# Kernel tuning notes

Hardware: AMD Instinct MI355X
Metric: run time of the kernel (lower is better)

Reference implementation:

```python
import jax, jax.numpy as jnp
import numpy as np

N = 2048   # nodes
E = 65536  # edges (avg degree 32)
F = 7      # node_feature_dim
S = 32     # state_dim
L = 16     # latent_dim
R = 3      # message passing rounds


def setup_inputs() -> dict:
    key = jax.random.key(0)
    ks = jax.random.split(key, 12)
    g = lambda k, shape, s: (jax.random.normal(k, shape, jnp.float32) * s)
    return dict(
        x=g(ks[0], (N, F), 1.0),
        edge_index=jax.random.randint(ks[1], (2, E), 0, N, dtype=jnp.int32),
        # input_net Linear(F->S)
        W_in=g(ks[2], (F, S), 0.3), b_in=jnp.zeros((S,), jnp.float32),
        # message nets: R x Linear(S->S)
        W_msg=g(ks[3], (R, S, S), 0.15), b_msg=jnp.zeros((R, S), jnp.float32),
        # GRU cells: R x (weight_ih, weight_hh) stored (in, 3*S) with torch gate order r,z,n
        W_ih=g(ks[4], (R, S, 3 * S), 0.15), W_hh=g(ks[5], (R, S, 3 * S), 0.15),
        b_ih=jnp.zeros((R, 3 * S), jnp.float32), b_hh=jnp.zeros((R, 3 * S), jnp.float32),
        # mu / logstd heads Linear(S->L)
        W_mu=g(ks[6], (S, L), 0.15), b_mu=jnp.zeros((L,), jnp.float32),
        W_ls=g(ks[7], (S, L), 0.15), b_ls=jnp.zeros((L,), jnp.float32),
        # decoder: Linear(2L->L), ReLU, Linear(L->1)
        W_d1=g(ks[8], (2 * L, L), 0.2), b_d1=jnp.zeros((L,), jnp.float32),
        W_d2=g(ks[9], (L, 1), 0.2), b_d2=jnp.zeros((1,), jnp.float32),
    )


def reference(x, edge_index, W_in, b_in, W_msg, b_msg, W_ih, W_hh, b_ih, b_hh,
              W_mu, b_mu, W_ls, b_ls, W_d1, b_d1, W_d2, b_d2):
    src, dst = edge_index[0], edge_index[1]
    # encoder
    state = jax.nn.relu(x @ W_in + b_in)  # [N, S]
    for r in range(R):
        message = jax.nn.relu(state @ W_msg[r] + b_msg[r])          # [N, S]
        aggregated = jax.ops.segment_sum(jnp.take(message, src, axis=0), dst,
                                         num_segments=N)            # [N, S]
        # GRUCell(aggregated, state), torch gate order: r, z, n
        gx = aggregated @ W_ih[r] + b_ih[r]                         # [N, 3S]
        gh = state @ W_hh[r] + b_hh[r]                              # [N, 3S]
        xr, xz, xn = jnp.split(gx, 3, axis=-1)
        hr, hz, hn = jnp.split(gh, 3, axis=-1)
        rg = jax.nn.sigmoid(xr + hr)
        zg = jax.nn.sigmoid(xz + hz)
        ng = jnp.tanh(xn + rg * hn)
        new_h = (1.0 - zg) * ng + zg * state
        state = state + new_h
    mu = state @ W_mu + b_mu        # [N, L]
    logstd = state @ W_ls + b_ls    # [N, L]
    # eval-mode reparameterize: z = mu
    z = mu
    # decode: Linear on concat([z_i, z_j]) == z_i @ W_d1[:L] + z_j @ W_d1[L:]
    a = z @ W_d1[:L]   # [N, L] contribution of row latent
    b = z @ W_d1[L:]   # [N, L] contribution of col latent
    h = jax.nn.relu(a[:, None, :] + b[None, :, :] + b_d1)  # [N, N, L]
    adj_logits = (h @ W_d2)[..., 0] + b_d2[0]              # [N, N]
    adj_logits = (adj_logits + adj_logits.T) / 2.0
    adj_recon = jax.nn.sigmoid(adj_logits)
    return (adj_recon, mu, logstd)
```

## Files before the change

kernel.cpp:

```cpp
#include <hip/hip_runtime.h>
#include <math.h>

#define NN 2048
#define EE 65536
#define FF 7
#define SS 32
#define LL 16
#define BKT 64
#define OCAP 4096

__device__ __forceinline__ float fsig(float x) { return 1.f / (1.f + __expf(-x)); }
__device__ __forceinline__ float ftanh(float x) { return 1.f - 2.f / (__expf(2.f * x) + 1.f); }

__global__ void k_enc(const float* __restrict__ x,
                      const float* __restrict__ W_in, const float* __restrict__ b_in,
                      const float* __restrict__ Wm, const float* __restrict__ bm,
                      float* __restrict__ st_out, float* __restrict__ msgA,
                      float* __restrict__ msgB,
                      int* __restrict__ cnt, int* __restrict__ ocnt,
                      int* __restrict__ bucket) {
    int gid = blockIdx.x * 256 + threadIdx.x;
    bucket[gid] = NN;
    bucket[gid + 65536] = NN;
    if (gid < NN) cnt[gid] = 0;
    if (gid == 0) *ocnt = 0;
    if (gid < SS) { msgA[NN * SS + gid] = 0.f; msgB[NN * SS + gid] = 0.f; }

    int n = gid >> 5, s = gid & 31;
    const float* xr = x + n * FF;
    float acc = b_in[s];
#pragma unroll
    for (int k = 0; k < FF; k++) acc += xr[k] * W_in[k * SS + s];
    float st = fmaxf(acc, 0.f);
    st_out[n * SS + s] = st;
    float m = bm[s];
#pragma unroll
    for (int k = 0; k < SS; k++) m += __shfl(st, k, 32) * Wm[k * SS + s];
    msgA[n * SS + s] = fmaxf(m, 0.f);
}

__global__ void k_bucket(const int* __restrict__ ei, int* __restrict__ cnt,
                         int* __restrict__ ocnt, int* __restrict__ olist,
                         int* __restrict__ bucket) {
    int e = blockIdx.x * 256 + threadIdx.x;
    int src = ei[e], dst = ei[EE + e];
    int slot = atomicAdd(&cnt[dst], 1);
    if (slot < BKT) bucket[dst * BKT + slot] = src;
    else {
        int oi = atomicAdd(ocnt, 1);
        if (oi < OCAP) { olist[2 * oi] = src; olist[2 * oi + 1] = dst; }
    }
}

__device__ __forceinline__ float gather_gru(int n, int s,
        const int* __restrict__ cnt, const int* __restrict__ bucket,
        const int* __restrict__ ocnt, const int* __restrict__ olist,
        const float* __restrict__ msg_in, const float* __restrict__ st_in,
        const float* __restrict__ Wih, const float* __restrict__ Whh,
        const float* __restrict__ bih, const float* __restrict__ bhh) {
    const int* bk = bucket + n * BKT;
    int i0 = bk[s], i1 = bk[SS + s];
    float acc = 0.f;
#pragma unroll
    for (int k = 0; k < 32; k++) acc += msg_in[__shfl(i0, k, 32) * SS + s];
#pragma unroll
    for (int k = 0; k < 32; k++) acc += msg_in[__shfl(i1, k, 32) * SS + s];
    int deg = cnt[n];
    if (deg > BKT) {
        int oc = *ocnt; if (oc > OCAP) oc = OCAP;
        for (int i = 0; i < oc; i++)
            if (olist[2 * i + 1] == n) acc += msg_in[olist[2 * i] * SS + s];
    }
    float h0 = st_in[n * SS + s];
    float xr = bih[s], xz = bih[SS + s], xn = bih[2 * SS + s];
    float hr = bhh[s], hz = bhh[SS + s], hn = bhh[2 * SS + s];
#pragma unroll
    for (int k = 0; k < SS; k++) {
        float av = __shfl(acc, k, 32);
        float hv = __shfl(h0, k, 32);
        const float* wi = Wih + k * 3 * SS;
        const float* wh = Whh + k * 3 * SS;
        xr += av * wi[s];
        xz += av * wi[SS + s];
        xn += av * wi[2 * SS + s];
        hr += hv * wh[s];
        hz += hv * wh[SS + s];
        hn += hv * wh[2 * SS + s];
    }
    float rg = fsig(xr + hr);
    float zg = fsig(xz + hz);
    float ng = ftanh(xn + rg * hn);
    return h0 + (1.f - zg) * ng + zg * h0;
}

__global__ void k_round(const int* __restrict__ cnt, const int* __restrict__ bucket,
                        const int* __restrict__ ocnt, const int* __restrict__ olist,
                        const float* __restrict__ msg_in, const float* __restrict__ st_in,
                        const float* __restrict__ Wih, const float* __restrict__ Whh,
                        const float* __restrict__ bih, const float* __restrict__ bhh,
                        const float* __restrict__ Wm, const float* __restrict__ bm,
                        float* __restrict__ st_out, float* __restrict__ msg_out) {
    int gid = blockIdx.x * 256 + threadIdx.x;
    int n = gid >> 5, s = gid & 31;
    float st = gather_gru(n, s, cnt, bucket, ocnt, olist, msg_in, st_in,
                          Wih, Whh, bih, bhh);
    st_out[n * SS + s] = st;
    float mv = bm[s];
#pragma unroll
    for (int k = 0; k < SS; k++) mv += __shfl(st, k, 32) * Wm[k * SS + s];
    msg_out[n * SS + s] = fmaxf(mv, 0.f);
}

__global__ void k_final(const int* __restrict__ cnt, const int* __restrict__ bucket,
                        const int* __restrict__ ocnt, const int* __restrict__ olist,
                        const float* __restrict__ msg_in, const float* __restrict__ st_in,
                        const float* __restrict__ Wih, const float* __restrict__ Whh,
                        const float* __restrict__ bih, const float* __restrict__ bhh,
                        const float* __restrict__ W_mu, const float* __restrict__ b_mu,
                        const float* __restrict__ W_ls, const float* __restrict__ b_ls,
                        const float* __restrict__ W_d1, const float* __restrict__ b_d1,
                        float* __restrict__ out_mu, float* __restrict__ out_ls,
                        float* __restrict__ Abuf, float* __restrict__ Bbuf) {
    int gid = blockIdx.x * 256 + threadIdx.x;
    int n = gid >> 5, s = gid & 31;
    float st = gather_gru(n, s, cnt, bucket, ocnt, olist, msg_in, st_in,
                          Wih, Whh, bih, bhh);
    int l = s & 15;
    const float* W = (s < 16) ? W_mu : W_ls;
    float v = (s < 16) ? b_mu[l] : b_ls[l];
#pragma unroll
    for (int k = 0; k < SS; k++) v += __shfl(st, k, 32) * W[k * LL + l];
    if (s < 16) out_mu[n * LL + l] = v; else out_ls[n * LL + l] = v;
    const float* Wd = W_d1 + ((s < 16) ? 0 : LL * LL);
    float ab = (s < 16) ? b_d1[l] : 0.f;
#pragma unroll
    for (int k = 0; k < LL; k++) ab += __shfl(v, k, 32) * Wd[k * LL + l];
    if (s < 16) Abuf[n * LL + l] = ab; else Bbuf[n * LL + l] = ab;
}

__global__ __launch_bounds__(256) void dec_kernel(const float* __restrict__ Abuf,
                                                  const float* __restrict__ Bbuf,
                                                  const float* __restrict__ W_d2,
                                                  const float* __restrict__ b_d2,
                                                  float* __restrict__ out) {
    __shared__ float ldsAj[LL * 64];
    __shared__ float ldsBj[LL * 64];
    __shared__ float ldsT[64 * 65];
    int t = blockIdx.x;
    int bi = (int)((65.f - sqrtf(4225.f - 8.f * (float)t)) * 0.5f);
    if (bi < 0) bi = 0;
    if (bi > 31) bi = 31;
    while (bi > 0 && (65 * bi - bi * bi) / 2 > t) bi--;
    while (bi < 31 && (65 * (bi + 1) - (bi + 1) * (bi + 1)) / 2 <= t) bi++;
    int bj = bi + (t - (65 * bi - bi * bi) / 2);
    int i0 = bi * 64, j0 = bj * 64;
    int tid = threadIdx.x;

    {
        int jr = tid >> 2, q = tid & 3;
        float4 va = ((const float4*)(Abuf + (size_t)(j0 + jr) * LL))[q];
        float4 vb = ((const float4*)(Bbuf + (size_t)(j0 + jr) * LL))[q];
        int l4 = q * 4;
        ldsAj[(l4 + 0) * 64 + jr] = va.x; ldsAj[(l4 + 1) * 64 + jr] = va.y;
        ldsAj[(l4 + 2) * 64 + jr] = va.z; ldsAj[(l4 + 3) * 64 + jr] = va.w;
        ldsBj[(l4 + 0) * 64 + jr] = vb.x; ldsBj[(l4 + 1) * 64 + jr] = vb.y;
        ldsBj[(l4 + 2) * 64 + jr] = vb.z; ldsBj[(l4 + 3) * 64 + jr] = vb.w;
    }
    __syncthreads();

    int jo = tid & 63;
    int ig = tid >> 6;
    float aj[LL], bjr[LL], w[LL];
#pragma unroll
    for (int l = 0; l < LL; l++) {
        aj[l] = ldsAj[l * 64 + jo];
        bjr[l] = ldsBj[l * 64 + jo];
        w[l] = W_d2[l];
    }
    float bd2 = b_d2[0];
    int j = j0 + jo;

#pragma unroll 2
    for (int ii = 0; ii < 16; ii++) {
        int i = i0 + ig * 16 + ii;
        const float4* Ai4 = (const float4*)(Abuf + (size_t)i * LL);
        const float4* Bi4 = (const float4*)(Bbuf + (size_t)i * LL);
        float4 a0 = Ai4[0], a1 = Ai4[1], a2 = Ai4[2], a3 = Ai4[3];
        float4 b0 = Bi4[0], b1 = Bi4[1], b2 = Bi4[2], b3 = Bi4[3];
        float ai[LL] = {a0.x, a0.y, a0.z, a0.w, a1.x, a1.y, a1.z, a1.w,
                        a2.x, a2.y, a2.z, a2.w, a3.x, a3.y, a3.z, a3.w};
        float bi_[LL] = {b0.x, b0.y, b0.z, b0.w, b1.x, b1.y, b1.z, b1.w,
                         b2.x, b2.y, b2.z, b2.w, b3.x, b3.y, b3.z, b3.w};
        float accij = 0.f, accji = 0.f;
#pragma unroll
        for (int l = 0; l < LL; l++) {
            accij += w[l] * fmaxf(ai[l] + bjr[l], 0.f);
            accji += w[l] * fmaxf(aj[l] + bi_[l], 0.f);
        }
        float logit = 0.5f * (accij + accji) + bd2;
        float p = 1.f / (1.f + __expf(-logit));
        out[(size_t)i * NN + j] = p;
        ldsT[jo * 65 + ig * 16 + ii] = p;
    }

    if (bi != bj) {
        __syncthreads();
        int jj = tid >> 2, qi = tid & 3;
        float v[16];
#pragma unroll
        for (int m = 0; m < 16; m++) v[m] = ldsT[jj * 65 + qi * 16 + m];
        float4* dst = (float4*)(out + (size_t)(j0 + jj) * NN + i0 + qi * 16);
#pragma unroll
        for (int q4 = 0; q4 < 4; q4++)
            dst[q4] = make_float4(v[4 * q4], v[4 * q4 + 1], v[4 * q4 + 2], v[4 * q4 + 3]);
    }
}

extern "C" void kernel_launch(void* const* d_in, const int* in_sizes, int n_in,
                              void* d_out, int out_size, void* d_ws, size_t ws_size,
                              hipStream_t stream) {
    const float* x    = (const float*)d_in[0];
    const int*   ei   = (const int*)d_in[1];
    const float* W_in = (const float*)d_in[2];
    const float* b_in = (const float*)d_in[3];
    const float* W_msg = (const float*)d_in[4];
    const float* b_msg = (const float*)d_in[5];
    const float* W_ih = (const float*)d_in[6];
    const float* W_hh = (const float*)d_in[7];
    const float* b_ih = (const float*)d_in[8];
    const float* b_hh = (const float*)d_in[9];
    const float* W_mu = (const float*)d_in[10];
    const float* b_mu = (const float*)d_in[11];
    const float* W_ls = (const float*)d_in[12];
    const float* b_ls = (const float*)d_in[13];
    const float* W_d1 = (const float*)d_in[14];
    const float* b_d1 = (const float*)d_in[15];
    const float* W_d2 = (const float*)d_in[16];
    const float* b_d2 = (const float*)d_in[17];

    float* ws = (float*)d_ws;
    float* stA  = ws;
    float* stB  = stA + NN * SS;
    float* msgA = stB + NN * SS;
    float* msgB = msgA + (NN + 1) * SS;
    float* Abuf = msgB + (NN + 1) * SS;
    float* Bbuf = Abuf + NN * LL;
    int* cnt    = (int*)(Bbuf + NN * LL);
    int* ocnt   = cnt + NN;
    int* olist  = ocnt + 1;
    int* bucket = olist + 2 * OCAP;

    float* out_adj = (float*)d_out;
    float* out_mu  = out_adj + (size_t)NN * NN;
    float* out_ls  = out_mu + NN * LL;

    k_enc<<<256, 256, 0, stream>>>(x, W_in, b_in, W_msg, b_msg,
                                   stA, msgA, msgB, cnt, ocnt, bucket);
    k_bucket<<<EE / 256, 256, 0, stream>>>(ei, cnt, ocnt, olist, bucket);

    k_round<<<256, 256, 0, stream>>>(
        cnt, bucket, ocnt, olist, msgA, stA, W_ih, W_hh, b_ih, b_hh,
        W_msg + 1 * SS * SS, b_msg + 1 * SS, stB, msgB);
    k_round<<<256, 256, 0, stream>>>(
        cnt, bucket, ocnt, olist, msgB, stB,
        W_ih + SS * 3 * SS, W_hh + SS * 3 * SS, b_ih + 3 * SS, b_hh + 3 * SS,
        W_msg + 2 * SS * SS, b_msg + 2 * SS, stA, msgA);
    k_final<<<256, 256, 0, stream>>>(
        cnt, bucket, ocnt, olist, msgA, stA,
        W_ih + 2 * SS * 3 * SS, W_hh + 2 * SS * 3 * SS,
        b_ih + 2 * 3 * SS, b_hh + 2 * 3 * SS,
        W_mu, b_mu, W_ls, b_ls, W_d1, b_d1,
        out_mu, out_ls, Abuf, Bbuf);

    dec_kernel<<<528, 256, 0, stream>>>(Abuf, Bbuf, W_d2, b_d2, out_adj);
}
```

Measured before the change: 56.11 us.

## Fuse all stages into one cooperative kernel with grid syncs

Replaces six separate kernel launches with a single cooperative kernel of 256 blocks that uses grid-wide syncs between the encoder, edge bucketing, the three GRU rounds and the decoder. The decoder now loops over its 528 tiles with a stride of 256 blocks. Bucket slots are no longer pre-filled with a sentinel that points at a zero row. Instead, gather reads are masked by node degree, which also removes the extra zero row from the message buffers. The aim is to cut launch gaps and inter-kernel drain. The cost is grid-sync overhead, and the decoder phase has fewer blocks than tiles, so parallelism there is reduced.

```diff
diff --git a/kernel.cpp b/kernel.cpp
--- a/kernel.cpp
+++ b/kernel.cpp
@@ -1,5 +1,8 @@
 #include <hip/hip_runtime.h>
+#include <hip/hip_cooperative_groups.h>
 #include <math.h>
+
+namespace cg = cooperative_groups;
 
 #define NN 2048
 #define EE 65536
@@ -9,63 +12,41 @@
 #define BKT 64
 #define OCAP 4096
 
+struct Params {
+    const float *x; const int *ei;
+    const float *W_in, *b_in, *W_msg, *b_msg, *W_ih, *W_hh, *b_ih, *b_hh;
+    const float *W_mu, *b_mu, *W_ls, *b_ls, *W_d1, *b_d1, *W_d2, *b_d2;
+    float *stA, *stB, *msgA, *msgB, *Abuf, *Bbuf;
+    int *cnt, *ocnt, *olist, *bucket;
+    float *out_adj, *out_mu, *out_ls;
+};
+
 __device__ __forceinline__ float fsig(float x) { return 1.f / (1.f + __expf(-x)); }
 __device__ __forceinline__ float ftanh(float x) { return 1.f - 2.f / (__expf(2.f * x) + 1.f); }
 
-__global__ void k_enc(const float* __restrict__ x,
-                      const float* __restrict__ W_in, const float* __restrict__ b_in,
-                      const float* __restrict__ Wm, const float* __restrict__ bm,
-                      float* __restrict__ st_out, float* __restrict__ msgA,
-                      float* __restrict__ msgB,
-                      int* __restrict__ cnt, int* __restrict__ ocnt,
-                      int* __restrict__ bucket) {
-    int gid = blockIdx.x * 256 + threadIdx.x;
-    bucket[gid] = NN;
-    bucket[gid + 65536] = NN;
-    if (gid < NN) cnt[gid] = 0;
-    if (gid == 0) *ocnt = 0;
-    if (gid < SS) { msgA[NN * SS + gid] = 0.f; msgB[NN * SS + gid] = 0.f; }
-
-    int n = gid >> 5, s = gid & 31;
-    const float* xr = x + n * FF;
-    float acc = b_in[s];
-#pragma unroll
-    for (int k = 0; k < FF; k++) acc += xr[k] * W_in[k * SS + s];
-    float st = fmaxf(acc, 0.f);
-    st_out[n * SS + s] = st;
-    float m = bm[s];
-#pragma unroll
-    for (int k = 0; k < SS; k++) m += __shfl(st, k, 32) * Wm[k * SS + s];
-    msgA[n * SS + s] = fmaxf(m, 0.f);
-}
-
-__global__ void k_bucket(const int* __restrict__ ei, int* __restrict__ cnt,
-                         int* __restrict__ ocnt, int* __restrict__ olist,
-                         int* __restrict__ bucket) {
-    int e = blockIdx.x * 256 + threadIdx.x;
-    int src = ei[e], dst = ei[EE + e];
-    int slot = atomicAdd(&cnt[dst], 1);
-    if (slot < BKT) bucket[dst * BKT + slot] = src;
-    else {
-        int oi = atomicAdd(ocnt, 1);
-        if (oi < OCAP) { olist[2 * oi] = src; olist[2 * oi + 1] = dst; }
-    }
-}
-
-__device__ __forceinline__ float gather_gru(int n, int s,
-        const int* __restrict__ cnt, const int* __restrict__ bucket,
-        const int* __restrict__ ocnt, const int* __restrict__ olist,
-        const float* __restrict__ msg_in, const float* __restrict__ st_in,
-        const float* __restrict__ Wih, const float* __restrict__ Whh,
-        const float* __restrict__ bih, const float* __restrict__ bhh) {
+__device__ __forceinline__ float gather_gru(int n, int s, int deg,
+        const int* bucket, const int* ocnt, const int* olist,
+        const float* msg_in, const float* st_in,
+        const float* Wih, const float* Whh,
+        const float* bih, const float* bhh) {
     const int* bk = bucket + n * BKT;
     int i0 = bk[s], i1 = bk[SS + s];
     float acc = 0.f;
 #pragma unroll
-    for (int k = 0; k < 32; k++) acc += msg_in[__shfl(i0, k, 32) * SS + s];
-#pragma unroll
-    for (int k = 0; k < 32; k++) acc += msg_in[__shfl(i1, k, 32) * SS + s];
-    int deg = cnt[n];
+    for (int k = 0; k < 32; k++) {
+        int bsrc = __shfl(i0, k, 32);
+        int src = (k < deg) ? bsrc : 0;
+        float v = msg_in[src * SS + s];
+        acc += (k < deg) ? v : 0.f;
+    }
+#pragma unroll
+    for (int k = 0; k < 32; k++) {
+        int kk = 32 + k;
+        int bsrc = __shfl(i1, k, 32);
+        int src = (kk < deg) ? bsrc : 0;
+        float v = msg_in[src * SS + s];
+        acc += (kk < deg) ? v : 0.f;
+    }
     if (deg > BKT) {
         int oc = *ocnt; if (oc > OCAP) oc = OCAP;
         for (int i = 0; i < oc; i++)
@@ -93,184 +74,204 @@
     return h0 + (1.f - zg) * ng + zg * h0;
 }
 
-__global__ void k_round(const int* __restrict__ cnt, const int* __restrict__ bucket,
-                        const int* __restrict__ ocnt, const int* __restrict__ olist,
-                        const float* __restrict__ msg_in, const float* __restrict__ st_in,
-                        const float* __restrict__ Wih, const float* __restrict__ Whh,
-                        const float* __restrict__ bih, const float* __restrict__ bhh,
-                        const float* __restrict__ Wm, const float* __restrict__ bm,
-                        float* __restrict__ st_out, float* __restrict__ msg_out) {
-    int gid = blockIdx.x * 256 + threadIdx.x;
-    int n = gid >> 5, s = gid & 31;
-    float st = gather_gru(n, s, cnt, bucket, ocnt, olist, msg_in, st_in,
-                          Wih, Whh, bih, bhh);
-    st_out[n * SS + s] = st;
-    float mv = bm[s];
-#pragma unroll
-    for (int k = 0; k < SS; k++) mv += __shfl(st, k, 32) * Wm[k * SS + s];
-    msg_out[n * SS + s] = fmaxf(mv, 0.f);
-}
-
-__global__ void k_final(const int* __restrict__ cnt, const int* __restrict__ bucket,
-                        const int* __restrict__ ocnt, const int* __restrict__ olist,
-                        const float* __restrict__ msg_in, const float* __restrict__ st_in,
-                        const float* __restrict__ Wih, const float* __restrict__ Whh,
-                        const float* __restrict__ bih, const float* __restrict__ bhh,
-                        const float* __restrict__ W_mu, const float* __restrict__ b_mu,
-                        const float* __restrict__ W_ls, const float* __restrict__ b_ls,
-                        const float* __restrict__ W_d1, const float* __restrict__ b_d1,
-                        float* __restrict__ out_mu, float* __restrict__ out_ls,
-                        float* __restrict__ Abuf, float* __restrict__ Bbuf) {
-    int gid = blockIdx.x * 256 + threadIdx.x;
-    int n = gid >> 5, s = gid & 31;
-    float st = gather_gru(n, s, cnt, bucket, ocnt, olist, msg_in, st_in,
-                          Wih, Whh, bih, bhh);
-    int l = s & 15;
-    const float* W = (s < 16) ? W_mu : W_ls;
-    float v = (s < 16) ? b_mu[l] : b_ls[l];
-#pragma unroll
-    for (int k = 0; k < SS; k++) v += __shfl(st, k, 32) * W[k * LL + l];
-    if (s < 16) out_mu[n * LL + l] = v; else out_ls[n * LL + l] = v;
-    const float* Wd = W_d1 + ((s < 16) ? 0 : LL * LL);
-    float ab = (s < 16) ? b_d1[l] : 0.f;
-#pragma unroll
-    for (int k = 0; k < LL; k++) ab += __shfl(v, k, 32) * Wd[k * LL + l];
-    if (s < 16) Abuf[n * LL + l] = ab; else Bbuf[n * LL + l] = ab;
-}
-
-__global__ __launch_bounds__(256) void dec_kernel(const float* __restrict__ Abuf,
-                                                  const float* __restrict__ Bbuf,
-                                                  const float* __restrict__ W_d2,
-                                                  const float* __restrict__ b_d2,
-                                                  float* __restrict__ out) {
+__global__ void __launch_bounds__(256) fused(Params p) {
+    cg::grid_group grid = cg::this_grid();
     __shared__ float ldsAj[LL * 64];
     __shared__ float ldsBj[LL * 64];
     __shared__ float ldsT[64 * 65];
-    int t = blockIdx.x;
-    int bi = (int)((65.f - sqrtf(4225.f - 8.f * (float)t)) * 0.5f);
-    if (bi < 0) bi = 0;
-    if (bi > 31) bi = 31;
-    while (bi > 0 && (65 * bi - bi * bi) / 2 > t) bi--;
-    while (bi < 31 && (65 * (bi + 1) - (bi + 1) * (bi + 1)) / 2 <= t) bi++;
-    int bj = bi + (t - (65 * bi - bi * bi) / 2);
-    int i0 = bi * 64, j0 = bj * 64;
+
     int tid = threadIdx.x;
-
-    {
-        int jr = tid >> 2, q = tid & 3;
-        float4 va = ((const float4*)(Abuf + (size_t)(j0 + jr) * LL))[q];
-        float4 vb = ((const float4*)(Bbuf + (size_t)(j0 + jr) * LL))[q];
-        int l4 = q * 4;
-        ldsAj[(l4 + 0) * 64 + jr] = va.x; ldsAj[(l4 + 1) * 64 + jr] = va.y;
-        ldsAj[(l4 + 2) * 64 + jr] = va.z; ldsAj[(l4 + 3) * 64 + jr] = va.w;
-        ldsBj[(l4 + 0) * 64 + jr] = vb.x; ldsBj[(l4 + 1) * 64 + jr] = vb.y;
-        ldsBj[(l4 + 2) * 64 + jr] = vb.z; ldsBj[(l4 + 3) * 64 + jr] = vb.w;
-    }
-    __syncthreads();
-
-    int jo = tid & 63;
-    int ig = tid >> 6;
-    float aj[LL], bjr[LL], w[LL];
-#pragma unroll
-    for (int l = 0; l < LL; l++) {
-        aj[l] = ldsAj[l * 64 + jo];
-        bjr[l] = ldsBj[l * 64 + jo];
-        w[l] = W_d2[l];
-    }
-    float bd2 = b_d2[0];
-    int j = j0 + jo;
+    int gid = blockIdx.x * 256 + tid;
+    int n = gid >> 5, s = gid & 31;
+
+    {
+        const float* xr = p.x + n * FF;
+        float acc = p.b_in[s];
+#pragma unroll
+        for (int k = 0; k < FF; k++) acc += xr[k] * p.W_in[k * SS + s];
+        float st = fmaxf(acc, 0.f);
+        p.stA[n * SS + s] = st;
+        float m = p.b_msg[s];
+#pragma unroll
+        for (int k = 0; k < SS; k++) m += __shfl(st, k, 32) * p.W_msg[k * SS + s];
+        p.msgA[n * SS + s] = fmaxf(m, 0.f);
+        if (gid < NN) p.cnt[gid] = 0;
+        if (gid == 0) *p.ocnt = 0;
+    }
+    grid.sync();
+
+    {
+        int e = gid;
+        int src = p.ei[e], dst = p.ei[EE + e];
+        int slot = atomicAdd(&p.cnt[dst], 1);
+        if (slot < BKT) p.bucket[dst * BKT + slot] = src;
+        else {
+            int oi = atomicAdd(p.ocnt, 1);
+            if (oi < OCAP) { p.olist[2 * oi] = src; p.olist[2 * oi + 1] = dst; }
+        }
+    }
+    grid.sync();
+
+    int deg = p.cnt[n];
+
+    {
+        float st = gather_gru(n, s, deg, p.bucket, p.ocnt, p.olist, p.msgA, p.stA,
+                              p.W_ih, p.W_hh, p.b_ih, p.b_hh);
+        p.stB[n * SS + s] = st;
+        const float* Wm = p.W_msg + 1 * SS * SS;
+        const float* bm = p.b_msg + 1 * SS;
+        float mv = bm[s];
+#pragma unroll
+        for (int k = 0; k < SS; k++) mv += __shfl(st, k, 32) * Wm[k * SS + s];
+        p.msgB[n * SS + s] = fmaxf(mv, 0.f);
+    }
+    grid.sync();
+
+    {
+        float st = gather_gru(n, s, deg, p.bucket, p.ocnt, p.olist, p.msgB, p.stB,
+                              p.W_ih + SS * 3 * SS, p.W_hh + SS * 3 * SS,
+                              p.b_ih + 3 * SS, p.b_hh + 3 * SS);
+        p.stA[n * SS + s] = st;
+        const float* Wm = p.W_msg + 2 * SS * SS;
+        const float* bm = p.b_msg + 2 * SS;
+        float mv = bm[s];
+#pragma unroll
+        for (int k = 0; k < SS; k++) mv += __shfl(st, k, 32) * Wm[k * SS + s];
+        p.msgA[n * SS + s] = fmaxf(mv, 0.f);
+    }
+    grid.sync();
+
+    {
+        float st = gather_gru(n, s, deg, p.bucket, p.ocnt, p.olist, p.msgA, p.stA,
+                              p.W_ih + 2 * SS * 3 * SS, p.W_hh + 2 * SS * 3 * SS,
+                              p.b_ih + 2 * 3 * SS, p.b_hh + 2 * 3 * SS);
+        int l = s & 15;
+        const float* W = (s < 16) ? p.W_mu : p.W_ls;
+        float v = (s < 16) ? p.b_mu[l] : p.b_ls[l];
+#pragma unroll
+        for (int k = 0; k < SS; k++) v += __shfl(st, k, 32) * W[k * LL + l];
+        if (s < 16) p.out_mu[n * LL + l] = v; else p.out_ls[n * LL + l] = v;
+        const float* Wd = p.W_d1 + ((s < 16) ? 0 : LL * LL);
+        float ab = (s < 16) ? p.b_d1[l] : 0.f;
+#pragma unroll
+        for (int k = 0; k < LL; k++) ab += __shfl(v, k, 32) * Wd[k * LL + l];
+        if (s < 16) p.Abuf[n * LL + l] = ab; else p.Bbuf[n * LL + l] = ab;
+    }
+    grid.sync();
+
+    float w[LL];
+#pragma unroll
+    for (int l = 0; l < LL; l++) w[l] = p.W_d2[l];
+    float bd2 = p.b_d2[0];
+
+    for (int t = blockIdx.x; t < 528; t += 256) {
+        __syncthreads();
+        int bi = (int)((65.f - sqrtf(4225.f - 8.f * (float)t)) * 0.5f);
+        if (bi < 0) bi = 0;
+        if (bi > 31) bi = 31;
+        while (bi > 0 && (65 * bi - bi * bi) / 2 > t) bi--;
+        while (bi < 31 && (65 * (bi + 1) - (bi + 1) * (bi + 1)) / 2 <= t) bi++;
+        int bj = bi + (t - (65 * bi - bi * bi) / 2);
+        int i0 = bi * 64, j0 = bj * 64;
+
+        {
+            int jr = tid >> 2, q = tid & 3;
+            float4 va = ((const float4*)(p.Abuf + (size_t)(j0 + jr) * LL))[q];
+            float4 vb = ((const float4*)(p.Bbuf + (size_t)(j0 + jr) * LL))[q];
+            int l4 = q * 4;
+            ldsAj[(l4 + 0) * 64 + jr] = va.x; ldsAj[(l4 + 1) * 64 + jr] = va.y;
+            ldsAj[(l4 + 2) * 64 + jr] = va.z; ldsAj[(l4 + 3) * 64 + jr] = va.w;
+            ldsBj[(l4 + 0) * 64 + jr] = vb.x; ldsBj[(l4 + 1) * 64 + jr] = vb.y;
+            ldsBj[(l4 + 2) * 64 + jr] = vb.z; ldsBj[(l4 + 3) * 64 + jr] = vb.w;
+        }
+        __syncthreads();
+
+        int jo = tid & 63;
+        int ig = tid >> 6;
+        float aj[LL], bjr[LL];
+#pragma unroll
+        for (int l = 0; l < LL; l++) {
+            aj[l] = ldsAj[l * 64 + jo];
+            bjr[l] = ldsBj[l * 64 + jo];
+        }
+        int j = j0 + jo;
 
 #pragma unroll 2
-    for (int ii = 0; ii < 16; ii++) {
-        int i = i0 + ig * 16 + ii;
-        const float4* Ai4 = (const float4*)(Abuf + (size_t)i * LL);
-        const float4* Bi4 = (const float4*)(Bbuf + (size_t)i * LL);
-        float4 a0 = Ai4[0], a1 = Ai4[1], a2 = Ai4[2], a3 = Ai4[3];
-        float4 b0 = Bi4[0], b1 = Bi4[1], b2 = Bi4[2], b3 = Bi4[3];
-        float ai[LL] = {a0.x, a0.y, a0.z, a0.w, a1.x, a1.y, a1.z, a1.w,
-                        a2.x, a2.y, a2.z, a2.w, a3.x, a3.y, a3.z, a3.w};
-        float bi_[LL] = {b0.x, b0.y, b0.z, b0.w, b1.x, b1.y, b1.z, b1.w,
-                         b2.x, b2.y, b2.z, b2.w, b3.x, b3.y, b3.z, b3.w};
-        float accij = 0.f, accji = 0.f;
-#pragma unroll
-        for (int l = 0; l < LL; l++) {
-            accij += w[l] * fmaxf(ai[l] + bjr[l], 0.f);
-            accji += w[l] * fmaxf(aj[l] + bi_[l], 0.f);
-        }
-        float logit = 0.5f * (accij + accji) + bd2;
-        float p = 1.f / (1.f + __expf(-logit));
-        out[(size_t)i * NN + j] = p;
-        ldsT[jo * 65 + ig * 16 + ii] = p;
-    }
-
-    if (bi != bj) {
-        __syncthreads();
-        int jj = tid >> 2, qi = tid & 3;
-        float v[16];
-#pragma unroll
-        for (int m = 0; m < 16; m++) v[m] = ldsT[jj * 65 + qi * 16 + m];
-        float4* dst = (float4*)(out + (size_t)(j0 + jj) * NN + i0 + qi * 16);
-#pragma unroll
-        for (int q4 = 0; q4 < 4; q4++)
-            dst[q4] = make_float4(v[4 * q4], v[4 * q4 + 1], v[4 * q4 + 2], v[4 * q4 + 3]);
+        for (int ii = 0; ii < 16; ii++) {
+            int i = i0 + ig * 16 + ii;
+            const float4* Ai4 = (const float4*)(p.Abuf + (size_t)i * LL);
+            const float4* Bi4 = (const float4*)(p.Bbuf + (size_t)i * LL);
+            float4 a0 = Ai4[0], a1 = Ai4[1], a2 = Ai4[2], a3 = Ai4[3];
+            float4 b0 = Bi4[0], b1 = Bi4[1], b2 = Bi4[2], b3 = Bi4[3];
+            float ai[LL] = {a0.x, a0.y, a0.z, a0.w, a1.x, a1.y, a1.z, a1.w,
+                            a2.x, a2.y, a2.z, a2.w, a3.x, a3.y, a3.z, a3.w};
+            float bi_[LL] = {b0.x, b0.y, b0.z, b0.w, b1.x, b1.y, b1.z, b1.w,
+                             b2.x, b2.y, b2.z, b2.w, b3.x, b3.y, b3.z, b3.w};
+            float accij = 0.f, accji = 0.f;
+#pragma unroll
+            for (int l = 0; l < LL; l++) {
+                accij += w[l] * fmaxf(ai[l] + bjr[l], 0.f);
+                accji += w[l] * fmaxf(aj[l] + bi_[l], 0.f);
+            }
+            float logit = 0.5f * (accij + accji) + bd2;
+            float pr = 1.f / (1.f + __expf(-logit));
+            p.out_adj[(size_t)i * NN + j] = pr;
+            ldsT[jo * 65 + ig * 16 + ii] = pr;
+        }
+
+        if (bi != bj) {
+            __syncthreads();
+            int jj = tid >> 2, qi = tid & 3;
+            float v[16];
+#pragma unroll
+            for (int m = 0; m < 16; m++) v[m] = ldsT[jj * 65 + qi * 16 + m];
+            float4* dst = (float4*)(p.out_adj + (size_t)(j0 + jj) * NN + i0 + qi * 16);
+#pragma unroll
+            for (int q4 = 0; q4 < 4; q4++)
+                dst[q4] = make_float4(v[4 * q4], v[4 * q4 + 1], v[4 * q4 + 2], v[4 * q4 + 3]);
+        }
     }
 }
 
 extern "C" void kernel_launch(void* const* d_in, const int* in_sizes, int n_in,
                               void* d_out, int out_size, void* d_ws, size_t ws_size,
                               hipStream_t stream) {
-    const float* x    = (const float*)d_in[0];
-    const int*   ei   = (const int*)d_in[1];
-    const float* W_in = (const float*)d_in[2];
-    const float* b_in = (const float*)d_in[3];
-    const float* W_msg = (const float*)d_in[4];
-    const float* b_msg = (const float*)d_in[5];
-    const float* W_ih = (const float*)d_in[6];
-    const float* W_hh = (const float*)d_in[7];
-    const float* b_ih = (const float*)d_in[8];
-    const float* b_hh = (const float*)d_in[9];
-    const float* W_mu = (const float*)d_in[10];
-    const float* b_mu = (const float*)d_in[11];
-    const float* W_ls = (const float*)d_in[12];
-    const float* b_ls = (const float*)d_in[13];
-    const float* W_d1 = (const float*)d_in[14];
-    const float* b_d1 = (const float*)d_in[15];
-    const float* W_d2 = (const float*)d_in[16];
-    const float* b_d2 = (const float*)d_in[17];
+    Params p;
+    p.x     = (const float*)d_in[0];
+    p.ei    = (const int*)d_in[1];
+    p.W_in  = (const float*)d_in[2];
+    p.b_in  = (const float*)d_in[3];
+    p.W_msg = (const float*)d_in[4];
+    p.b_msg = (const float*)d_in[5];
+    p.W_ih  = (const float*)d_in[6];
+    p.W_hh  = (const float*)d_in[7];
+    p.b_ih  = (const float*)d_in[8];
+    p.b_hh  = (const float*)d_in[9];
+    p.W_mu  = (const float*)d_in[10];
+    p.b_mu  = (const float*)d_in[11];
+    p.W_ls  = (const float*)d_in[12];
+    p.b_ls  = (const float*)d_in[13];
+    p.W_d1  = (const float*)d_in[14];
+    p.b_d1  = (const float*)d_in[15];
+    p.W_d2  = (const float*)d_in[16];
+    p.b_d2  = (const float*)d_in[17];
 
     float* ws = (float*)d_ws;
-    float* stA  = ws;
-    float* stB  = stA + NN * SS;
-    float* msgA = stB + NN * SS;
-    float* msgB = msgA + (NN + 1) * SS;
-    float* Abuf = msgB + (NN + 1) * SS;
-    float* Bbuf = Abuf + NN * LL;
-    int* cnt    = (int*)(Bbuf + NN * LL);
-    int* ocnt   = cnt + NN;
-    int* olist  = ocnt + 1;
-    int* bucket = olist + 2 * OCAP;
-
-    float* out_adj = (float*)d_out;
-    float* out_mu  = out_adj + (size_t)NN * NN;
-    float* out_ls  = out_mu + NN * LL;
-
-    k_enc<<<256, 256, 0, stream>>>(x, W_in, b_in, W_msg, b_msg,
-                                   stA, msgA, msgB, cnt, ocnt, bucket);
-    k_bucket<<<EE / 256, 256, 0, stream>>>(ei, cnt, ocnt, olist, bucket);
-
-    k_round<<<256, 256, 0, stream>>>(
-        cnt, bucket, ocnt, olist, msgA, stA, W_ih, W_hh, b_ih, b_hh,
-        W_msg + 1 * SS * SS, b_msg + 1 * SS, stB, msgB);
-    k_round<<<256, 256, 0, stream>>>(
-        cnt, bucket, ocnt, olist, msgB, stB,
-        W_ih + SS * 3 * SS, W_hh + SS * 3 * SS, b_ih + 3 * SS, b_hh + 3 * SS,
-        W_msg + 2 * SS * SS, b_msg + 2 * SS, stA, msgA);
-    k_final<<<256, 256, 0, stream>>>(
-        cnt, bucket, ocnt, olist, msgA, stA,
-        W_ih + 2 * SS * 3 * SS, W_hh + 2 * SS * 3 * SS,
-        b_ih + 2 * 3 * SS, b_hh + 2 * 3 * SS,
-        W_mu, b_mu, W_ls, b_ls, W_d1, b_d1,
-        out_mu, out_ls, Abuf, Bbuf);
-
-    dec_kernel<<<528, 256, 0, stream>>>(Abuf, Bbuf, W_d2, b_d2, out_adj);
+    p.stA  = ws;
+    p.stB  = p.stA + NN * SS;
+    p.msgA = p.stB + NN * SS;
+    p.msgB = p.msgA + NN * SS;
+    p.Abuf = p.msgB + NN * SS;
+    p.Bbuf = p.Abuf + NN * LL;
+    p.cnt  = (int*)(p.Bbuf + NN * LL);
+    p.ocnt = p.cnt + NN;
+    p.olist = p.ocnt + 1;
+    p.bucket = p.olist + 2 * OCAP;
+
+    p.out_adj = (float*)d_out;
+    p.out_mu  = p.out_adj + (size_t)NN * NN;
+    p.out_ls  = p.out_mu + NN * LL;
+
+    void* args[] = { &p };
+    hipLaunchCooperativeKernel((const void*)fused, dim3(256), dim3(256), args, 0, stream);
 }
```

New measurement: 206.8 us. +268.6%, slower.
